# Optimization experiments

Measured on AMD Instinct MI355X. Metric: run time of the kernel, lower is better.

Reference implementation:

```python
import jax, jax.numpy as jnp
import numpy as np

N_NODES = 50000
N_EDGES = 500000
IN_CH = 128
OUT_CH = 128
N_TYPES = 2
NEG_SLOPE = 0.2
EPS = 1e-16


def setup_inputs() -> dict:
    key = jax.random.key(0)
    ks = jax.random.split(key, 8)
    x = jax.random.normal(ks[0], (N_NODES, IN_CH), dtype=jnp.float32)
    edge_index = jax.random.randint(ks[1], (2, N_EDGES), 0, N_NODES, dtype=jnp.int64)
    edge_type = jax.random.randint(ks[2], (N_EDGES,), 0, N_TYPES, dtype=jnp.int64)
    # xavier-uniform-like params
    def xav(k, shape, fan_in, fan_out):
        lim = np.sqrt(6.0 / (fan_in + fan_out)).astype(np.float32)
        return jax.random.uniform(k, shape, jnp.float32, -lim, lim)
    weight = xav(ks[3], (N_TYPES, IN_CH, OUT_CH), IN_CH, OUT_CH)
    att = xav(ks[4], (N_TYPES, 2 * OUT_CH), N_TYPES, 2 * OUT_CH)
    root_w = xav(ks[5], (OUT_CH, IN_CH), IN_CH, OUT_CH)
    lim = 1.0 / np.sqrt(IN_CH)
    root_b = jax.random.uniform(ks[6], (OUT_CH,), jnp.float32, -lim, lim)
    return {"x": x, "edge_index": edge_index, "edge_type": edge_type,
            "weight": weight, "att": att, "root_w": root_w, "root_b": root_b}


def reference(x, edge_index, edge_type, weight, att, root_w, root_b):
    n = x.shape[0]
    src, dst = edge_index[0], edge_index[1]
    # Per-edge transform x[src] @ W[edge_type] == gather from per-type node transforms
    h_all = jnp.einsum('ni,tio->nto', x, weight)          # [N, T, O]
    h_src = h_all[src, edge_type]                          # [E, O]
    h_dst = h_all[dst, edge_type]                          # [E, O]
    a = att[edge_type]                                     # [E, 2O]
    o = h_src.shape[1]
    e = (h_src * a[:, :o]).sum(-1) + (h_dst * a[:, o:]).sum(-1)
    e = jnp.where(e > 0, e, NEG_SLOPE * e)                 # leaky_relu
    # segment softmax over dst (stable: subtract per-segment max)
    seg_max = jax.ops.segment_max(e, dst, num_segments=n)
    ex = jnp.exp(e - seg_max[dst])
    denom = jax.ops.segment_sum(ex, dst, num_segments=n)
    alpha = ex / (denom[dst] + EPS)
    # dropout is identity in eval mode
    msg = h_src * alpha[:, None]
    out = jax.ops.segment_sum(msg, dst, num_segments=n)
    out = out + x @ root_w.T + root_b
    return out
```

## Files before the change

kernel.cpp:

```cpp
#include <hip/hip_runtime.h>
#include <hip/hip_bf16.h>

#define N_NODES 50000
#define N_PAD 50048
#define N_EDGES 500000
#define IN_CH 128
#define OUT_CH 128
#define NEG_SLOPE 0.2f
#define EPS_F 1e-16f

typedef __attribute__((ext_vector_type(8))) short bf16x8;
typedef __attribute__((ext_vector_type(4))) float f32x4;

__device__ __forceinline__ unsigned short bf16_rne(float f) {
    unsigned int u = __float_as_uint(f);
    u += 0x7FFFu + ((u >> 16) & 1u);
    return (unsigned short)(u >> 16);
}
__device__ __forceinline__ float bf16_to_f32(unsigned short h) {
    return __uint_as_float(((unsigned int)h) << 16);
}

#define XSWZ(n, k) ((size_t)(n) * 128 + ((k) ^ (((n) & 7) << 3)))
#define LSWZ(row, col) ((row) * 128 + ((col) ^ (((row) & 7) << 3)))

__device__ __forceinline__ void gload16(const unsigned short* g, unsigned short* l) {
    __builtin_amdgcn_global_load_lds(
        (const __attribute__((address_space(1))) unsigned int*)g,
        (__attribute__((address_space(3))) unsigned int*)l, 16, 0, 0);
}

__global__ __launch_bounds__(256) void prep_kernel(
    const float* __restrict__ x, const float* __restrict__ weight,
    const float* __restrict__ root_w,
    unsigned short* __restrict__ xhi, unsigned short* __restrict__ xlo,
    unsigned short* __restrict__ bt_hi, unsigned short* __restrict__ bt_lo)
{
    const int gid = blockIdx.x * 256 + threadIdx.x;
    const int gsz = gridDim.x * 256;

    const float4* xg = (const float4*)x;
    for (int i = gid; i < N_PAD * 32; i += gsz) {
        int n = i >> 5, c4 = i & 31;
        float4 v = make_float4(0.f, 0.f, 0.f, 0.f);
        if (n < N_NODES) v = xg[(size_t)n * 32 + c4];
        unsigned short h0 = bf16_rne(v.x), h1 = bf16_rne(v.y),
                       h2 = bf16_rne(v.z), h3 = bf16_rne(v.w);
        ushort4 hh = make_ushort4(h0, h1, h2, h3);
        ushort4 ll = make_ushort4(bf16_rne(v.x - bf16_to_f32(h0)),
                                  bf16_rne(v.y - bf16_to_f32(h1)),
                                  bf16_rne(v.z - bf16_to_f32(h2)),
                                  bf16_rne(v.w - bf16_to_f32(h3)));
        size_t off = XSWZ(n, c4 * 4);
        *(ushort4*)&xhi[off] = hh;
        *(ushort4*)&xlo[off] = ll;
    }

    for (int i = gid; i < 384 * 128; i += gsz) {
        int n = i >> 7, k = i & 127;
        float v;
        if (n < 256) {
            int t = n >> 7, o = n & 127;
            v = weight[(size_t)t * 16384 + (size_t)k * 128 + o];
        } else {
            v = root_w[(size_t)(n - 256) * 128 + k];
        }
        unsigned short h = bf16_rne(v);
        bt_hi[i] = h;
        bt_lo[i] = bf16_rne(v - bf16_to_f32(h));
    }
}

#define MBLK 391

__global__ __launch_bounds__(256, 2) void mfma_gemm_kernel(
    const unsigned short* __restrict__ xhi,
    const unsigned short* __restrict__ xlo,
    const unsigned short* __restrict__ bt_hi,
    const unsigned short* __restrict__ bt_lo,
    const float* __restrict__ att, const float* __restrict__ root_b,
    float* __restrict__ hall, float* __restrict__ out,
    float* __restrict__ sL, float* __restrict__ sR)
{
    __shared__ unsigned short Ah[128 * 128];
    __shared__ unsigned short Al[128 * 128];
    __shared__ float sLds[128][2];

    const int tid = threadIdx.x;
    const int lane = tid & 63;
    const int w = tid >> 6;
    const int bid = blockIdx.x;
    const int c = bid / MBLK;
    const int m0 = (bid - c * MBLK) * 128;

    if (tid < 128) { sLds[tid][0] = 0.f; sLds[tid][1] = 0.f; }

    {
        const unsigned short* srch = xhi + (size_t)m0 * 128;
        const unsigned short* srcl = xlo + (size_t)m0 * 128;
        #pragma unroll
        for (int it = 0; it < 8; ++it) {
            int base = it * 2048 + w * 512;
            gload16(srch + base + lane * 8, &Ah[base]);
            gload16(srcl + base + lane * 8, &Al[base]);
        }
    }
    __syncthreads();

    const int mh = (w >> 1) * 64;
    const int nh = (w & 1) * 64;
    const int lr = lane & 15;
    const int lk = (lane >> 4) * 8;

    const unsigned short* bh_base =
        bt_hi + ((size_t)(c * 128 + nh + lr)) * 128 + lk;
    const unsigned short* bl_base =
        bt_lo + ((size_t)(c * 128 + nh + lr)) * 128 + lk;

    f32x4 acc[4][4];
    #pragma unroll
    for (int mi = 0; mi < 4; ++mi)
        #pragma unroll
        for (int ni = 0; ni < 4; ++ni)
            acc[mi][ni] = (f32x4){0.f, 0.f, 0.f, 0.f};

    #pragma unroll
    for (int ks = 0; ks < 4; ++ks) {
        const int ko = ks * 32 + lk;
        bf16x8 bh[4], bl[4];
        #pragma unroll
        for (int ni = 0; ni < 4; ++ni) {
            bh[ni] = *(const bf16x8*)(bh_base + ni * 2048 + ks * 32);
            bl[ni] = *(const bf16x8*)(bl_base + ni * 2048 + ks * 32);
        }
        bf16x8 ah[4], al[4];
        #pragma unroll
        for (int mi = 0; mi < 4; ++mi) {
            int off = LSWZ(mh + mi * 16 + lr, ko);
            ah[mi] = *(const bf16x8*)&Ah[off];
            al[mi] = *(const bf16x8*)&Al[off];
        }
        #pragma unroll
        for (int mi = 0; mi < 4; ++mi)
            #pragma unroll
            for (int ni = 0; ni < 4; ++ni) {
                acc[mi][ni] = __builtin_amdgcn_mfma_f32_16x16x32_bf16(
                    ah[mi], bh[ni], acc[mi][ni], 0, 0, 0);
                acc[mi][ni] = __builtin_amdgcn_mfma_f32_16x16x32_bf16(
                    ah[mi], bl[ni], acc[mi][ni], 0, 0, 0);
                acc[mi][ni] = __builtin_amdgcn_mfma_f32_16x16x32_bf16(
                    al[mi], bh[ni], acc[mi][ni], 0, 0, 0);
            }
    }

    const int crow = (lane >> 4) * 4;
    const int ccol = lane & 15;
    if (c < 2) {
        #pragma unroll
        for (int mi = 0; mi < 4; ++mi)
            #pragma unroll
            for (int j = 0; j < 4; ++j) {
                int gm = m0 + mh + mi * 16 + crow + j;
                if (gm < N_NODES) {
                    #pragma unroll
                    for (int ni = 0; ni < 4; ++ni) {
                        int n = nh + ni * 16 + ccol;
                        hall[((size_t)gm * 2 + c) * 128 + n] = acc[mi][ni][j];
                    }
                }
            }
        float attLv[4], attRv[4];
        #pragma unroll
        for (int ni = 0; ni < 4; ++ni) {
            attLv[ni] = att[c * 256 + nh + ni * 16 + ccol];
            attRv[ni] = att[c * 256 + 128 + nh + ni * 16 + ccol];
        }
        #pragma unroll
        for (int mi = 0; mi < 4; ++mi)
            #pragma unroll
            for (int j = 0; j < 4; ++j) {
                float pL = acc[mi][0][j] * attLv[0] + acc[mi][1][j] * attLv[1]
                         + acc[mi][2][j] * attLv[2] + acc[mi][3][j] * attLv[3];
                float pR = acc[mi][0][j] * attRv[0] + acc[mi][1][j] * attRv[1]
                         + acc[mi][2][j] * attRv[2] + acc[mi][3][j] * attRv[3];
                #pragma unroll
                for (int off = 1; off < 16; off <<= 1) {
                    pL += __shfl_xor(pL, off);
                    pR += __shfl_xor(pR, off);
                }
                if (ccol == 0) {
                    int rl = mh + mi * 16 + crow + j;
                    atomicAdd(&sLds[rl][0], pL);
                    atomicAdd(&sLds[rl][1], pR);
                }
            }
        __syncthreads();
        if (tid < 128) {
            sL[(size_t)(m0 + tid) * 2 + c] = sLds[tid][0];
            sR[(size_t)(m0 + tid) * 2 + c] = sLds[tid][1];
        }
    } else {
        float rbv[4];
        #pragma unroll
        for (int ni = 0; ni < 4; ++ni) rbv[ni] = root_b[nh + ni * 16 + ccol];
        #pragma unroll
        for (int mi = 0; mi < 4; ++mi)
            #pragma unroll
            for (int j = 0; j < 4; ++j) {
                int gm = m0 + mh + mi * 16 + crow + j;
                if (gm < N_NODES) {
                    #pragma unroll
                    for (int ni = 0; ni < 4; ++ni) {
                        int n = nh + ni * 16 + ccol;
                        out[(size_t)gm * 128 + n] = acc[mi][ni][j] + rbv[ni];
                    }
                }
            }
    }
}

__global__ __launch_bounds__(256) void hist_kernel(
    const int* __restrict__ ei, int* __restrict__ deg)
{
    int i = blockIdx.x * 256 + threadIdx.x;
    if (i < N_EDGES) atomicAdd(&deg[ei[N_EDGES + i]], 1);
}

__global__ __launch_bounds__(256) void scan1_kernel(
    const int* __restrict__ deg, int* __restrict__ rp, int* __restrict__ bsum)
{
    __shared__ int s[256];
    int i = blockIdx.x * 256 + threadIdx.x;
    int v = (i < N_NODES) ? deg[i] : 0;
    s[threadIdx.x] = v;
    __syncthreads();
    #pragma unroll
    for (int off = 1; off < 256; off <<= 1) {
        int t = (threadIdx.x >= off) ? s[threadIdx.x - off] : 0;
        __syncthreads();
        s[threadIdx.x] += t;
        __syncthreads();
    }
    if (i < N_NODES) rp[i + 1] = s[threadIdx.x];
    if (threadIdx.x == 255) bsum[blockIdx.x] = s[255];
    if (i == 0) rp[0] = 0;
}

__global__ __launch_bounds__(256) void scan23_kernel(
    int* __restrict__ rp, const int* __restrict__ bsum, int nb)
{
    __shared__ int bl[256];
    int tid = threadIdx.x;
    bl[tid] = (tid < nb && tid < (int)blockIdx.x) ? bsum[tid] : 0;
    __syncthreads();
    #pragma unroll
    for (int off = 128; off; off >>= 1) {
        if (tid < off) bl[tid] += bl[tid + off];
        __syncthreads();
    }
    int pre = bl[0];
    int i = blockIdx.x * 256 + tid;
    if (i < N_NODES) rp[i + 1] += pre;
}

__global__ __launch_bounds__(256) void csr_scatter_kernel(
    const int* __restrict__ ei, const int* __restrict__ etype,
    const int* __restrict__ rp, int* __restrict__ cursor, int* __restrict__ skey)
{
    int i = blockIdx.x * 256 + threadIdx.x;
    if (i >= N_EDGES) return;
    int dst = ei[N_EDGES + i];
    int pos = rp[dst] + atomicAdd(&cursor[dst], 1);
    skey[pos] = (ei[i] << 1) | (etype[i] & 1);
}

__global__ __launch_bounds__(256) void node_agg_kernel(
    const int* __restrict__ rp, const int* __restrict__ skey,
    const float* __restrict__ hall,
    const float* __restrict__ sL, const float* __restrict__ sR,
    float* __restrict__ out)
{
    const int lane = threadIdx.x & 63;
    const int node = (blockIdx.x * 256 + threadIdx.x) >> 6;
    if (node >= N_NODES) return;
    const int r0 = rp[node], r1 = rp[node + 1];
    if (r0 == r1) return;

    const float sR0 = sR[(size_t)node * 2 + 0];
    const float sR1 = sR[(size_t)node * 2 + 1];
    const float NINF = -__builtin_inff();

    float mloc = NINF;
    for (int j = r0 + lane; j < r1; j += 64) {
        int key = skey[j], t = key & 1;
        float e = sL[(size_t)(key >> 1) * 2 + t] + (t ? sR1 : sR0);
        e = (e > 0.f) ? e : NEG_SLOPE * e;
        mloc = fmaxf(mloc, e);
    }
    #pragma unroll
    for (int off = 32; off; off >>= 1) mloc = fmaxf(mloc, __shfl_xor(mloc, off));

    const int sl = lane & 31;
    const int half = lane >> 5;
    float denom = 0.f;
    float4 acc = make_float4(0.f, 0.f, 0.f, 0.f);

    for (int j = r0 + half; j < r1; j += 4) {
        const int j2 = j + 2;
        const bool v2 = j2 < r1;
        const int k1 = skey[j];
        const int k2 = skey[v2 ? j2 : j];
        const int t1 = k1 & 1, t2 = k2 & 1;

        float e1 = sL[(size_t)(k1 >> 1) * 2 + t1] + (t1 ? sR1 : sR0);
        float e2 = sL[(size_t)(k2 >> 1) * 2 + t2] + (t2 ? sR1 : sR0);
        e1 = (e1 > 0.f) ? e1 : NEG_SLOPE * e1;
        e2 = (e2 > 0.f) ? e2 : NEG_SLOPE * e2;
        const float w1 = __expf(e1 - mloc);
        const float w2 = v2 ? __expf(e2 - mloc) : 0.f;

        const float4 h1 = *(const float4*)&hall[((size_t)(k1 >> 1) * 2 + t1) * 128 + sl * 4];
        const float4 h2 = *(const float4*)&hall[((size_t)(k2 >> 1) * 2 + t2) * 128 + sl * 4];

        denom += w1 + w2;
        acc.x += w1 * h1.x + w2 * h2.x;
        acc.y += w1 * h1.y + w2 * h2.y;
        acc.z += w1 * h1.z + w2 * h2.z;
        acc.w += w1 * h1.w + w2 * h2.w;
    }

    denom += __shfl_xor(denom, 32);
    acc.x += __shfl_xor(acc.x, 32);
    acc.y += __shfl_xor(acc.y, 32);
    acc.z += __shfl_xor(acc.z, 32);
    acc.w += __shfl_xor(acc.w, 32);

    if (half == 0) {
        const float inv = 1.f / (denom + EPS_F);
        float4* op = (float4*)&out[(size_t)node * 128 + sl * 4];
        float4 o = *op;
        o.x += acc.x * inv;
        o.y += acc.y * inv;
        o.z += acc.z * inv;
        o.w += acc.w * inv;
        *op = o;
    }
}

extern "C" void kernel_launch(void* const* d_in, const int* in_sizes, int n_in,
                              void* d_out, int out_size, void* d_ws, size_t ws_size,
                              hipStream_t stream) {
    const float* x      = (const float*)d_in[0];
    const int*   ei     = (const int*)d_in[1];
    const int*   etype  = (const int*)d_in[2];
    const float* weight = (const float*)d_in[3];
    const float* att    = (const float*)d_in[4];
    const float* root_w = (const float*)d_in[5];
    const float* root_b = (const float*)d_in[6];
    float* out = (float*)d_out;

    float* ws = (float*)d_ws;
    float* hall   = ws;
    float* sL     = hall + (size_t)N_NODES * 2 * 128;
    float* sR     = sL + (size_t)N_PAD * 2;
    int*   deg    = (int*)(sR + (size_t)N_PAD * 2);
    int*   cursor = deg + N_PAD;
    int*   rp     = cursor + N_PAD;
    int*   bsum   = rp + 50056;
    int*   skey   = bsum + 256;
    unsigned short* xhi   = (unsigned short*)(skey + N_EDGES);
    unsigned short* xlo   = xhi + (size_t)N_PAD * 128;
    unsigned short* bt_hi = xlo + (size_t)N_PAD * 128;
    unsigned short* bt_lo = bt_hi + 384 * 128;

    const int NB_E = (N_EDGES + 255) / 256;
    const int NB_N = (N_NODES + 255) / 256;

    hipMemsetAsync(deg, 0, sizeof(int) * (size_t)N_PAD * 2, stream);

    prep_kernel<<<2048, 256, 0, stream>>>(x, weight, root_w, xhi, xlo, bt_hi, bt_lo);

    mfma_gemm_kernel<<<3 * MBLK, 256, 0, stream>>>(
        xhi, xlo, bt_hi, bt_lo, att, root_b, hall, out, sL, sR);

    hist_kernel<<<NB_E, 256, 0, stream>>>(ei, deg);
    scan1_kernel<<<NB_N, 256, 0, stream>>>(deg, rp, bsum);
    scan23_kernel<<<NB_N, 256, 0, stream>>>(rp, bsum, NB_N);
    csr_scatter_kernel<<<NB_E, 256, 0, stream>>>(ei, etype, rp, cursor, skey);

    node_agg_kernel<<<(N_NODES + 3) / 4, 256, 0, stream>>>(
        rp, skey, hall, sL, sR, out);
}
```

Before: 243.5 us.

## Store per-type node features in bf16, halve GEMM tiles, fold histogram into prep

The per-type transformed node features (hall) are now rounded to bf16 when written and widened back to fp32 in the aggregation kernel. This halves the bytes of the dominant random gather per edge. The GEMM tile shrinks from 128 to 64 rows, with twice the blocks and a higher occupancy bound. The degree histogram is folded into the prep kernel to drop one launch. The trade-off is lost precision in the messages, since hall was previously full fp32.

```diff
diff --git a/kernel.cpp b/kernel.cpp
--- a/kernel.cpp
+++ b/kernel.cpp
@@ -4,8 +4,6 @@
 #define N_NODES 50000
 #define N_PAD 50048
 #define N_EDGES 500000
-#define IN_CH 128
-#define OUT_CH 128
 #define NEG_SLOPE 0.2f
 #define EPS_F 1e-16f
 
@@ -20,6 +18,10 @@
 __device__ __forceinline__ float bf16_to_f32(unsigned short h) {
     return __uint_as_float(((unsigned int)h) << 16);
 }
+__device__ __forceinline__ float4 bf4_to_f4(ushort4 u) {
+    return make_float4(bf16_to_f32(u.x), bf16_to_f32(u.y),
+                       bf16_to_f32(u.z), bf16_to_f32(u.w));
+}
 
 #define XSWZ(n, k) ((size_t)(n) * 128 + ((k) ^ (((n) & 7) << 3)))
 #define LSWZ(row, col) ((row) * 128 + ((col) ^ (((row) & 7) << 3)))
@@ -32,9 +34,10 @@
 
 __global__ __launch_bounds__(256) void prep_kernel(
     const float* __restrict__ x, const float* __restrict__ weight,
-    const float* __restrict__ root_w,
+    const float* __restrict__ root_w, const int* __restrict__ ei,
     unsigned short* __restrict__ xhi, unsigned short* __restrict__ xlo,
-    unsigned short* __restrict__ bt_hi, unsigned short* __restrict__ bt_lo)
+    unsigned short* __restrict__ bt_hi, unsigned short* __restrict__ bt_lo,
+    int* __restrict__ deg)
 {
     const int gid = blockIdx.x * 256 + threadIdx.x;
     const int gsz = gridDim.x * 256;
@@ -69,37 +72,40 @@
         bt_hi[i] = h;
         bt_lo[i] = bf16_rne(v - bf16_to_f32(h));
     }
-}
-
-#define MBLK 391
-
-__global__ __launch_bounds__(256, 2) void mfma_gemm_kernel(
+
+    for (int i = gid; i < N_EDGES; i += gsz)
+        atomicAdd(&deg[ei[N_EDGES + i]], 1);
+}
+
+#define MBLK 782
+
+__global__ __launch_bounds__(256, 4) void mfma_gemm_kernel(
     const unsigned short* __restrict__ xhi,
     const unsigned short* __restrict__ xlo,
     const unsigned short* __restrict__ bt_hi,
     const unsigned short* __restrict__ bt_lo,
     const float* __restrict__ att, const float* __restrict__ root_b,
-    float* __restrict__ hall, float* __restrict__ out,
+    unsigned short* __restrict__ hall, float* __restrict__ out,
     float* __restrict__ sL, float* __restrict__ sR)
 {
-    __shared__ unsigned short Ah[128 * 128];
-    __shared__ unsigned short Al[128 * 128];
-    __shared__ float sLds[128][2];
+    __shared__ unsigned short Ah[64 * 128];
+    __shared__ unsigned short Al[64 * 128];
+    __shared__ float sLds[64][2];
 
     const int tid = threadIdx.x;
     const int lane = tid & 63;
     const int w = tid >> 6;
     const int bid = blockIdx.x;
     const int c = bid / MBLK;
-    const int m0 = (bid - c * MBLK) * 128;
-
-    if (tid < 128) { sLds[tid][0] = 0.f; sLds[tid][1] = 0.f; }
+    const int m0 = (bid - c * MBLK) * 64;
+
+    if (tid < 64) { sLds[tid][0] = 0.f; sLds[tid][1] = 0.f; }
 
     {
         const unsigned short* srch = xhi + (size_t)m0 * 128;
         const unsigned short* srcl = xlo + (size_t)m0 * 128;
         #pragma unroll
-        for (int it = 0; it < 8; ++it) {
+        for (int it = 0; it < 4; ++it) {
             int base = it * 2048 + w * 512;
             gload16(srch + base + lane * 8, &Ah[base]);
             gload16(srcl + base + lane * 8, &Al[base]);
@@ -107,7 +113,7 @@
     }
     __syncthreads();
 
-    const int mh = (w >> 1) * 64;
+    const int mh = (w >> 1) * 32;
     const int nh = (w & 1) * 64;
     const int lr = lane & 15;
     const int lk = (lane >> 4) * 8;
@@ -117,9 +123,9 @@
     const unsigned short* bl_base =
         bt_lo + ((size_t)(c * 128 + nh + lr)) * 128 + lk;
 
-    f32x4 acc[4][4];
-    #pragma unroll
-    for (int mi = 0; mi < 4; ++mi)
+    f32x4 acc[2][4];
+    #pragma unroll
+    for (int mi = 0; mi < 2; ++mi)
         #pragma unroll
         for (int ni = 0; ni < 4; ++ni)
             acc[mi][ni] = (f32x4){0.f, 0.f, 0.f, 0.f};
@@ -133,15 +139,15 @@
             bh[ni] = *(const bf16x8*)(bh_base + ni * 2048 + ks * 32);
             bl[ni] = *(const bf16x8*)(bl_base + ni * 2048 + ks * 32);
         }
-        bf16x8 ah[4], al[4];
-        #pragma unroll
-        for (int mi = 0; mi < 4; ++mi) {
+        bf16x8 ah[2], al[2];
+        #pragma unroll
+        for (int mi = 0; mi < 2; ++mi) {
             int off = LSWZ(mh + mi * 16 + lr, ko);
             ah[mi] = *(const bf16x8*)&Ah[off];
             al[mi] = *(const bf16x8*)&Al[off];
         }
         #pragma unroll
-        for (int mi = 0; mi < 4; ++mi)
+        for (int mi = 0; mi < 2; ++mi)
             #pragma unroll
             for (int ni = 0; ni < 4; ++ni) {
                 acc[mi][ni] = __builtin_amdgcn_mfma_f32_16x16x32_bf16(
@@ -157,7 +163,7 @@
     const int ccol = lane & 15;
     if (c < 2) {
         #pragma unroll
-        for (int mi = 0; mi < 4; ++mi)
+        for (int mi = 0; mi < 2; ++mi)
             #pragma unroll
             for (int j = 0; j < 4; ++j) {
                 int gm = m0 + mh + mi * 16 + crow + j;
@@ -165,7 +171,7 @@
                     #pragma unroll
                     for (int ni = 0; ni < 4; ++ni) {
                         int n = nh + ni * 16 + ccol;
-                        hall[((size_t)gm * 2 + c) * 128 + n] = acc[mi][ni][j];
+                        hall[((size_t)gm * 2 + c) * 128 + n] = bf16_rne(acc[mi][ni][j]);
                     }
                 }
             }
@@ -176,7 +182,7 @@
             attRv[ni] = att[c * 256 + 128 + nh + ni * 16 + ccol];
         }
         #pragma unroll
-        for (int mi = 0; mi < 4; ++mi)
+        for (int mi = 0; mi < 2; ++mi)
             #pragma unroll
             for (int j = 0; j < 4; ++j) {
                 float pL = acc[mi][0][j] * attLv[0] + acc[mi][1][j] * attLv[1]
@@ -195,7 +201,7 @@
                 }
             }
         __syncthreads();
-        if (tid < 128) {
+        if (tid < 64) {
             sL[(size_t)(m0 + tid) * 2 + c] = sLds[tid][0];
             sR[(size_t)(m0 + tid) * 2 + c] = sLds[tid][1];
         }
@@ -204,7 +210,7 @@
         #pragma unroll
         for (int ni = 0; ni < 4; ++ni) rbv[ni] = root_b[nh + ni * 16 + ccol];
         #pragma unroll
-        for (int mi = 0; mi < 4; ++mi)
+        for (int mi = 0; mi < 2; ++mi)
             #pragma unroll
             for (int j = 0; j < 4; ++j) {
                 int gm = m0 + mh + mi * 16 + crow + j;
@@ -219,13 +225,6 @@
     }
 }
 
-__global__ __launch_bounds__(256) void hist_kernel(
-    const int* __restrict__ ei, int* __restrict__ deg)
-{
-    int i = blockIdx.x * 256 + threadIdx.x;
-    if (i < N_EDGES) atomicAdd(&deg[ei[N_EDGES + i]], 1);
-}
-
 __global__ __launch_bounds__(256) void scan1_kernel(
     const int* __restrict__ deg, int* __restrict__ rp, int* __restrict__ bsum)
 {
@@ -276,7 +275,7 @@
 
 __global__ __launch_bounds__(256) void node_agg_kernel(
     const int* __restrict__ rp, const int* __restrict__ skey,
-    const float* __restrict__ hall,
+    const unsigned short* __restrict__ hall,
     const float* __restrict__ sL, const float* __restrict__ sR,
     float* __restrict__ out)
 {
@@ -319,8 +318,10 @@
         const float w1 = __expf(e1 - mloc);
         const float w2 = v2 ? __expf(e2 - mloc) : 0.f;
 
-        const float4 h1 = *(const float4*)&hall[((size_t)(k1 >> 1) * 2 + t1) * 128 + sl * 4];
-        const float4 h2 = *(const float4*)&hall[((size_t)(k2 >> 1) * 2 + t2) * 128 + sl * 4];
+        const ushort4 u1 = *(const ushort4*)&hall[((size_t)(k1 >> 1) * 2 + t1) * 128 + sl * 4];
+        const ushort4 u2 = *(const ushort4*)&hall[((size_t)(k2 >> 1) * 2 + t2) * 128 + sl * 4];
+        const float4 h1 = bf4_to_f4(u1);
+        const float4 h2 = bf4_to_f4(u2);
 
         denom += w1 + w2;
         acc.x += w1 * h1.x + w2 * h2.x;
@@ -359,15 +360,14 @@
     const float* root_b = (const float*)d_in[6];
     float* out = (float*)d_out;
 
-    float* ws = (float*)d_ws;
-    float* hall   = ws;
-    float* sL     = hall + (size_t)N_NODES * 2 * 128;
-    float* sR     = sL + (size_t)N_PAD * 2;
-    int*   deg    = (int*)(sR + (size_t)N_PAD * 2);
-    int*   cursor = deg + N_PAD;
-    int*   rp     = cursor + N_PAD;
-    int*   bsum   = rp + 50056;
-    int*   skey   = bsum + 256;
+    unsigned short* hall = (unsigned short*)d_ws;
+    float* sL   = (float*)(hall + (size_t)N_PAD * 2 * 128);
+    float* sR   = sL + (size_t)N_PAD * 2;
+    int* deg    = (int*)(sR + (size_t)N_PAD * 2);
+    int* cursor = deg + N_PAD;
+    int* rp     = cursor + N_PAD;
+    int* bsum   = rp + 50056;
+    int* skey   = bsum + 256;
     unsigned short* xhi   = (unsigned short*)(skey + N_EDGES);
     unsigned short* xlo   = xhi + (size_t)N_PAD * 128;
     unsigned short* bt_hi = xlo + (size_t)N_PAD * 128;
@@ -378,12 +378,12 @@
 
     hipMemsetAsync(deg, 0, sizeof(int) * (size_t)N_PAD * 2, stream);
 
-    prep_kernel<<<2048, 256, 0, stream>>>(x, weight, root_w, xhi, xlo, bt_hi, bt_lo);
+    prep_kernel<<<1024, 256, 0, stream>>>(x, weight, root_w, ei,
+                                          xhi, xlo, bt_hi, bt_lo, deg);
 
     mfma_gemm_kernel<<<3 * MBLK, 256, 0, stream>>>(
         xhi, xlo, bt_hi, bt_lo, att, root_b, hall, out, sL, sR);
 
-    hist_kernel<<<NB_E, 256, 0, stream>>>(ei, deg);
     scan1_kernel<<<NB_N, 256, 0, stream>>>(deg, rp, bsum);
     scan23_kernel<<<NB_N, 256, 0, stream>>>(rp, bsum, NB_N);
     csr_scatter_kernel<<<NB_E, 256, 0, stream>>>(ei, etype, rp, cursor, skey);
```

After: 233.7 us. 1.04x faster.
